# Performance work log

Measured on AMD Instinct MI355X. Metric: run time of the kernel, lower is better.

## Reference

```python
import jax, jax.numpy as jnp
import numpy as np

B = 16384
DENSE = 64
N_OH, N_MH = 8, 4
VOCAB = 100000
EMB = 32
HIST = 20
IN_DIM = DENSE + N_OH * EMB + N_MH * EMB  # 448
HID = [1024, 512, 256]
CROSS_ORDER = 4


def setup_inputs() -> dict:
    key = jax.random.key(0)
    ks = jax.random.split(key, 16)
    inp = {}
    inp['dense_x'] = jax.random.normal(ks[0], (B, DENSE), dtype=jnp.float32)
    inp['one_hot_x'] = jax.random.randint(ks[1], (B, N_OH), 0, VOCAB)
    inp['multi_hot_x'] = jax.random.randint(ks[2], (B, N_MH, HIST), 0, VOCAB)
    # embedding tables (one per field)
    inp['one_hot_emb'] = jax.random.normal(ks[3], (N_OH, VOCAB, EMB), dtype=jnp.float32) * 0.01
    inp['multi_hot_emb'] = jax.random.normal(ks[4], (N_MH, VOCAB, EMB), dtype=jnp.float32) * 0.01
    # cross layer params: w (in_dim,) per layer (xavier-like), b (in_dim,) zeros in torch init -> small random here
    inp['cross_w'] = jax.random.normal(ks[5], (CROSS_ORDER, IN_DIM), dtype=jnp.float32) * (6.0 / (IN_DIM + 1)) ** 0.5
    inp['cross_b'] = jnp.zeros((CROSS_ORDER, IN_DIM), dtype=jnp.float32)
    # deep net
    inp['W1'] = jax.random.normal(ks[6], (IN_DIM, HID[0]), dtype=jnp.float32) * (1.0 / IN_DIM) ** 0.5
    inp['b1'] = jnp.zeros((HID[0],), dtype=jnp.float32)
    inp['W2'] = jax.random.normal(ks[7], (HID[0], HID[1]), dtype=jnp.float32) * (1.0 / HID[0]) ** 0.5
    inp['b2'] = jnp.zeros((HID[1],), dtype=jnp.float32)
    inp['W3'] = jax.random.normal(ks[8], (HID[1], HID[2]), dtype=jnp.float32) * (1.0 / HID[1]) ** 0.5
    inp['b3'] = jnp.zeros((HID[2],), dtype=jnp.float32)
    inp['lin_w'] = jax.random.normal(ks[9], (IN_DIM + HID[2], 1), dtype=jnp.float32) * (1.0 / (IN_DIM + HID[2])) ** 0.5
    inp['lin_b'] = jnp.zeros((1,), dtype=jnp.float32)
    return inp


def _embed_concat(one_hot_x, multi_hot_x, one_hot_emb, multi_hot_emb):
    # per-field one-hot lookup: (B, N_OH, EMB)
    oh = jax.vmap(lambda tab, idx: tab[idx], in_axes=(0, 1), out_axes=1)(one_hot_emb, one_hot_x)
    # per-field multi-hot sum-pool: (B, N_MH, EMB)
    mh = jax.vmap(lambda tab, idx: tab[idx].sum(axis=1), in_axes=(0, 1), out_axes=1)(multi_hot_emb, multi_hot_x)
    b = one_hot_x.shape[0]
    return jnp.concatenate([oh.reshape(b, -1), mh.reshape(b, -1)], axis=1)


def _forward(dense_x, one_hot_x, multi_hot_x, one_hot_emb, multi_hot_emb,
             cross_w, cross_b, W1, b1, W2, b2, W3, b3, lin_w, lin_b):
    emb_x = _embed_concat(one_hot_x, multi_hot_x, one_hot_emb, multi_hot_emb)
    x0 = jnp.concatenate([dense_x, emb_x], axis=1)  # (B, IN_DIM)
    # CrossNet: (x0 xi^T) w == x0 * (xi . w); same math as torch bmm, O(d) form
    xi = x0
    for l in range(CROSS_ORDER):
        xi = x0 * (xi @ cross_w[l])[:, None] + cross_b[l] + xi
    # DeepNet
    h = jax.nn.relu(x0 @ W1 + b1)
    h = jax.nn.relu(h @ W2 + b2)
    h = jax.nn.relu(h @ W3 + b3)
    h_cat = jnp.concatenate([xi, h], axis=1)
    return jax.nn.sigmoid(h_cat @ lin_w + lin_b)  # (B, 1)


def reference(dense_x, one_hot_x, multi_hot_x, one_hot_emb, multi_hot_emb,
              cross_w, cross_b, W1, b1, W2, b2, W3, b3, lin_w, lin_b):
    return _forward(dense_x, one_hot_x, multi_hot_x, one_hot_emb, multi_hot_emb,
                    cross_w, cross_b, W1, b1, W2, b2, W3, b3, lin_w, lin_b)
```

## Files before the change

### kernel.cpp

```cpp
#include <hip/hip_runtime.h>
#include <hip/hip_bf16.h>
#include <math.h>

#define B_SZ 16384
#define DENSE 64
#define N_OH 8
#define N_MH 4
#define VOCAB 100000
#define EMB 32
#define HIST 20
#define IN_DIM 448
#define HID1 1024
#define HID2 512
#define HID3 256
#define CROSS_ORDER 4

typedef __bf16 bf16_t;
typedef __bf16 bf16x8 __attribute__((ext_vector_type(8)));
typedef __bf16 bf16x4 __attribute__((ext_vector_type(4)));
typedef float f32x16 __attribute__((ext_vector_type(16)));
typedef __attribute__((address_space(1))) const void cgvoid;
typedef __attribute__((address_space(3))) void lvoid;

#define S1 (IN_DIM * HID1)
#define S2 (HID1 * HID2)
#define S3 (HID2 * HID3)
#define EMB_BLOCKS (B_SZ / 4)
#define TR_BLOCKS ((S1 + S2 + S3 + 255) / 256)

__global__ __launch_bounds__(256) void embed_cross_transpose_kernel(
    const float* __restrict__ dense, const int* __restrict__ oh_idx,
    const int* __restrict__ mh_idx, const float* __restrict__ oh_emb,
    const float* __restrict__ mh_emb, const float* __restrict__ cw,
    const float* __restrict__ cb, const float* __restrict__ lw,
    const float* __restrict__ W1, const float* __restrict__ W2,
    const float* __restrict__ W3, bf16_t* __restrict__ T1,
    bf16_t* __restrict__ T2, bf16_t* __restrict__ T3,
    bf16_t* __restrict__ x0b, float* __restrict__ partial) {
  __shared__ float ldsAll[4 * IN_DIM];
  int bid = blockIdx.x;
  if (bid >= EMB_BLOCKS) {
    int idx = (bid - EMB_BLOCKS) * 256 + threadIdx.x;
    if (idx < S1) {
      int n = idx / IN_DIM, k = idx - n * IN_DIM;
      T1[idx] = (bf16_t)W1[(size_t)k * HID1 + n];
    } else if (idx < S1 + S2) {
      int i = idx - S1;
      int n = i / HID1, k = i - n * HID1;
      T2[i] = (bf16_t)W2[(size_t)k * HID2 + n];
    } else if (idx < S1 + S2 + S3) {
      int i = idx - S1 - S2;
      int n = i / HID2, k = i - n * HID2;
      T3[i] = (bf16_t)W3[(size_t)k * HID3 + n];
    }
    return;
  }
  int wv = threadIdx.x >> 6;
  int lane = threadIdx.x & 63;
  int row = bid * 4 + wv;
  float* L = ldsAll + wv * IN_DIM;

  L[lane] = dense[(size_t)row * DENSE + lane];

  {
    int f = lane >> 3, d4 = (lane & 7) * 4;
    int idx = oh_idx[row * N_OH + f];
    float4 ov = *reinterpret_cast<const float4*>(
        &oh_emb[((size_t)f * VOCAB + idx) * EMB + d4]);
    *reinterpret_cast<float4*>(&L[64 + lane * 4]) = ov;
  }

  {
    int f = lane >> 4, sub = lane & 15;
    int par = sub >> 3, d4 = (sub & 7) * 4;
    const int* hist = mh_idx + ((size_t)row * N_MH + f) * HIST;
    float4 ms = make_float4(0.f, 0.f, 0.f, 0.f);
#pragma unroll
    for (int jj = 0; jj < 10; ++jj) {
      int idx = hist[jj * 2 + par];
      float4 v = *reinterpret_cast<const float4*>(
          &mh_emb[((size_t)f * VOCAB + idx) * EMB + d4]);
      ms.x += v.x; ms.y += v.y; ms.z += v.z; ms.w += v.w;
    }
    ms.x += __shfl_xor(ms.x, 8);
    ms.y += __shfl_xor(ms.y, 8);
    ms.z += __shfl_xor(ms.z, 8);
    ms.w += __shfl_xor(ms.w, 8);
    if (par == 0)
      *reinterpret_cast<float4*>(&L[320 + f * 32 + (sub & 7) * 4]) = ms;
  }

  if (lane < 56) {
    float4 a = *reinterpret_cast<float4*>(&L[lane * 8]);
    float4 b = *reinterpret_cast<float4*>(&L[lane * 8 + 4]);
    bf16x8 o;
    o[0] = (bf16_t)a.x; o[1] = (bf16_t)a.y; o[2] = (bf16_t)a.z; o[3] = (bf16_t)a.w;
    o[4] = (bf16_t)b.x; o[5] = (bf16_t)b.y; o[6] = (bf16_t)b.z; o[7] = (bf16_t)b.w;
    *reinterpret_cast<bf16x8*>(x0b + (size_t)row * IN_DIM + lane * 8) = o;
  }

  float x0v[7], xiv[7];
#pragma unroll
  for (int r = 0; r < 7; ++r) {
    x0v[r] = L[lane + r * 64];
    xiv[r] = x0v[r];
  }
  for (int l = 0; l < CROSS_ORDER; ++l) {
    const float* w = cw + l * IN_DIM;
    const float* b = cb + l * IN_DIM;
    float dot = 0.f;
#pragma unroll
    for (int r = 0; r < 7; ++r) dot += xiv[r] * w[lane + r * 64];
#pragma unroll
    for (int s = 32; s > 0; s >>= 1) dot += __shfl_xor(dot, s);
#pragma unroll
    for (int r = 0; r < 7; ++r) xiv[r] = x0v[r] * dot + b[lane + r * 64] + xiv[r];
  }

  float s = 0.f;
#pragma unroll
  for (int r = 0; r < 7; ++r) s += xiv[r] * lw[lane + r * 64];
#pragma unroll
  for (int t = 32; t > 0; t >>= 1) s += __shfl_xor(s, t);
  if (lane == 0) partial[row] = s;
}

template <int N, int K, int GX, bool RELU>
__global__ __launch_bounds__(256) void gemm_bf16_kernel(
    const bf16_t* __restrict__ A, const bf16_t* __restrict__ Bt,
    const float* __restrict__ bias, bf16_t* __restrict__ C) {
  __shared__ bf16_t As[128 * 64];
  __shared__ bf16_t Bs[128 * 64];
  const int tid = threadIdx.x;
  const int lane = tid & 63;
  const int wid = tid >> 6;
  const int wr = wid >> 1;
  const int wc = wid & 1;

  const int nwg = gridDim.x;
  const int bid = blockIdx.x;
  const int swz = (bid & 7) * (nwg >> 3) + (bid >> 3);
  const int row0 = (swz / GX) * 128;
  const int col0 = (swz % GX) * 128;
  constexpr size_t Kb = (size_t)K * 2;

  const int l31 = lane & 31;
  const int lh = lane >> 5;

  const int strow = tid >> 3;
  const int stkb0 = (tid * 16) & 127;

  f32x16 acc[2][2];
#pragma unroll
  for (int m = 0; m < 2; ++m)
#pragma unroll
    for (int n = 0; n < 2; ++n)
#pragma unroll
      for (int r = 0; r < 16; ++r) acc[m][n][r] = 0.f;

  for (int k0 = 0; k0 < K; k0 += 64) {
    __syncthreads();
#pragma unroll
    for (int c = 0; c < 4; ++c) {
      int trow = c * 32 + strow;
      int skb = stkb0 ^ ((trow & 7) << 4);
      const char* gA = (const char*)A + (size_t)(row0 + trow) * Kb + (size_t)k0 * 2 + skb;
      const char* gB = (const char*)Bt + (size_t)(col0 + trow) * Kb + (size_t)k0 * 2 + skb;
      __builtin_amdgcn_global_load_lds((cgvoid*)gA,
          (lvoid*)((char*)As + c * 4096 + wid * 1024), 16, 0, 0);
      __builtin_amdgcn_global_load_lds((cgvoid*)gB,
          (lvoid*)((char*)Bs + c * 4096 + wid * 1024), 16, 0, 0);
    }
    __syncthreads();

#pragma unroll
    for (int kh = 0; kh < 4; ++kh) {
      const int koff = kh * 32 + lh * 16;
      bf16x8 a[2], b[2];
#pragma unroll
      for (int m = 0; m < 2; ++m) {
        int r = wr * 64 + m * 32 + l31;
        a[m] = *reinterpret_cast<const bf16x8*>(
            (const char*)As + r * 128 + (koff ^ ((r & 7) << 4)));
      }
#pragma unroll
      for (int n = 0; n < 2; ++n) {
        int ccol = wc * 64 + n * 32 + l31;
        b[n] = *reinterpret_cast<const bf16x8*>(
            (const char*)Bs + ccol * 128 + (koff ^ ((ccol & 7) << 4)));
      }
#pragma unroll
      for (int m = 0; m < 2; ++m)
#pragma unroll
        for (int n = 0; n < 2; ++n)
          acc[m][n] = __builtin_amdgcn_mfma_f32_32x32x16_bf16(a[m], b[n], acc[m][n], 0, 0, 0);
    }
  }

#pragma unroll
  for (int n = 0; n < 2; ++n) {
    int col = col0 + wc * 64 + n * 32 + l31;
    float bv = bias[col];
#pragma unroll
    for (int m = 0; m < 2; ++m) {
#pragma unroll
      for (int r = 0; r < 16; ++r) {
        int row = row0 + wr * 64 + m * 32 + (r & 3) + 8 * (r >> 2) + 4 * lh;
        float v = acc[m][n][r] + bv;
        if (RELU) v = fmaxf(v, 0.f);
        C[(size_t)row * N + col] = (bf16_t)v;
      }
    }
  }
}

__global__ __launch_bounds__(256) void final_kernel(
    const float* __restrict__ partial, const bf16_t* __restrict__ h3,
    const float* __restrict__ lw, const float* __restrict__ lb,
    float* __restrict__ out) {
  int wave = (blockIdx.x * blockDim.x + threadIdx.x) >> 6;
  int lane = threadIdx.x & 63;
  if (wave >= B_SZ) return;
  bf16x4 hv = *reinterpret_cast<const bf16x4*>(h3 + (size_t)wave * HID3 + lane * 4);
  float4 wv = *reinterpret_cast<const float4*>(lw + IN_DIM + lane * 4);
  float s = (float)hv[0] * wv.x + (float)hv[1] * wv.y +
            (float)hv[2] * wv.z + (float)hv[3] * wv.w;
#pragma unroll
  for (int t = 32; t > 0; t >>= 1) s += __shfl_xor(s, t);
  if (lane == 0) out[wave] = 1.f / (1.f + expf(-(s + partial[wave] + lb[0])));
}

extern "C" void kernel_launch(void* const* d_in, const int* in_sizes, int n_in,
                              void* d_out, int out_size, void* d_ws, size_t ws_size,
                              hipStream_t stream) {
  const float* dense = (const float*)d_in[0];
  const int* oh_idx = (const int*)d_in[1];
  const int* mh_idx = (const int*)d_in[2];
  const float* oh_emb = (const float*)d_in[3];
  const float* mh_emb = (const float*)d_in[4];
  const float* cw = (const float*)d_in[5];
  const float* cb = (const float*)d_in[6];
  const float* W1 = (const float*)d_in[7];
  const float* b1 = (const float*)d_in[8];
  const float* W2 = (const float*)d_in[9];
  const float* b2 = (const float*)d_in[10];
  const float* W3 = (const float*)d_in[11];
  const float* b3 = (const float*)d_in[12];
  const float* lw = (const float*)d_in[13];
  const float* lb = (const float*)d_in[14];
  float* out = (float*)d_out;

  char* p = (char*)d_ws;
  bf16_t* x0b = (bf16_t*)p;  p += (size_t)B_SZ * IN_DIM * 2;
  bf16_t* h1b = (bf16_t*)p;  p += (size_t)B_SZ * HID1 * 2;
  bf16_t* h2b = (bf16_t*)p;  p += (size_t)B_SZ * HID2 * 2;
  bf16_t* h3b = (bf16_t*)p;  p += (size_t)B_SZ * HID3 * 2;
  bf16_t* wT1 = (bf16_t*)p;  p += (size_t)HID1 * IN_DIM * 2;
  bf16_t* wT2 = (bf16_t*)p;  p += (size_t)HID2 * HID1 * 2;
  bf16_t* wT3 = (bf16_t*)p;  p += (size_t)HID2 * HID3 * 2;
  float* partial = (float*)p; p += (size_t)B_SZ * 4;

  embed_cross_transpose_kernel<<<EMB_BLOCKS + TR_BLOCKS, 256, 0, stream>>>(
      dense, oh_idx, mh_idx, oh_emb, mh_emb, cw, cb, lw,
      W1, W2, W3, wT1, wT2, wT3, x0b, partial);

  gemm_bf16_kernel<HID1, IN_DIM, HID1 / 128, true>
      <<<(B_SZ / 128) * (HID1 / 128), 256, 0, stream>>>(x0b, wT1, b1, h1b);
  gemm_bf16_kernel<HID2, HID1, HID2 / 128, true>
      <<<(B_SZ / 128) * (HID2 / 128), 256, 0, stream>>>(h1b, wT2, b2, h2b);
  gemm_bf16_kernel<HID3, HID2, HID3 / 128, true>
      <<<(B_SZ / 128) * (HID3 / 128), 256, 0, stream>>>(h2b, wT3, b3, h3b);

  final_kernel<<<B_SZ / 4, 256, 0, stream>>>(partial, h3b, lw, lb, out);
}
```

Baseline: 102.2 us.

## Fuse third GEMM with final linear projection and sigmoid

Replaces the third layer GEMM and the separate final kernel with one kernel. Each block computes a 64-row by full-256-column tile, applies bias and ReLU, dots with the linear weights in registers, reduces across lanes and waves through shared memory, and writes the sigmoid output. This removes the h3 round trip through global memory and one launch. In exchange it uses a different tile shape (64x256, 256 blocks), which may lower occupancy or MFMA efficiency for this layer.

```diff
diff --git a/kernel.cpp b/kernel.cpp
--- a/kernel.cpp
+++ b/kernel.cpp
@@ -17,7 +17,6 @@
 
 typedef __bf16 bf16_t;
 typedef __bf16 bf16x8 __attribute__((ext_vector_type(8)));
-typedef __bf16 bf16x4 __attribute__((ext_vector_type(4)));
 typedef float f32x16 __attribute__((ext_vector_type(16)));
 typedef __attribute__((address_space(1))) const void cgvoid;
 typedef __attribute__((address_space(3))) void lvoid;
@@ -125,7 +124,7 @@
   if (lane == 0) partial[row] = s;
 }
 
-template <int N, int K, int GX, bool RELU>
+template <int N, int K, int GX>
 __global__ __launch_bounds__(256) void gemm_bf16_kernel(
     const bf16_t* __restrict__ A, const bf16_t* __restrict__ Bt,
     const float* __restrict__ bias, bf16_t* __restrict__ C) {
@@ -206,28 +205,112 @@
 #pragma unroll
       for (int r = 0; r < 16; ++r) {
         int row = row0 + wr * 64 + m * 32 + (r & 3) + 8 * (r >> 2) + 4 * lh;
-        float v = acc[m][n][r] + bv;
-        if (RELU) v = fmaxf(v, 0.f);
+        float v = fmaxf(acc[m][n][r] + bv, 0.f);
         C[(size_t)row * N + col] = (bf16_t)v;
       }
     }
   }
 }
 
-__global__ __launch_bounds__(256) void final_kernel(
-    const float* __restrict__ partial, const bf16_t* __restrict__ h3,
-    const float* __restrict__ lw, const float* __restrict__ lb,
+__global__ __launch_bounds__(256) void gemm3_final_kernel(
+    const bf16_t* __restrict__ A,
+    const bf16_t* __restrict__ Bt,
+    const float* __restrict__ bias,
+    const float* __restrict__ lw,
+    const float* __restrict__ lb,
+    const float* __restrict__ partial,
     float* __restrict__ out) {
-  int wave = (blockIdx.x * blockDim.x + threadIdx.x) >> 6;
-  int lane = threadIdx.x & 63;
-  if (wave >= B_SZ) return;
-  bf16x4 hv = *reinterpret_cast<const bf16x4*>(h3 + (size_t)wave * HID3 + lane * 4);
-  float4 wv = *reinterpret_cast<const float4*>(lw + IN_DIM + lane * 4);
-  float s = (float)hv[0] * wv.x + (float)hv[1] * wv.y +
-            (float)hv[2] * wv.z + (float)hv[3] * wv.w;
-#pragma unroll
-  for (int t = 32; t > 0; t >>= 1) s += __shfl_xor(s, t);
-  if (lane == 0) out[wave] = 1.f / (1.f + expf(-(s + partial[wave] + lb[0])));
+  constexpr int K = HID2;
+  __shared__ bf16_t As[64 * 64];
+  __shared__ bf16_t Bs[256 * 64];
+  __shared__ float rowsum[64][2];
+  const int tid = threadIdx.x;
+  const int lane = tid & 63;
+  const int wid = tid >> 6;
+  const int wr = wid >> 1;
+  const int wc = wid & 1;
+  const int nwg = gridDim.x;
+  const int bid = blockIdx.x;
+  const int swz = (bid & 7) * (nwg >> 3) + (bid >> 3);
+  const int row0 = swz * 64;
+  constexpr size_t Kb = (size_t)K * 2;
+
+  const int l31 = lane & 31;
+  const int lh = lane >> 5;
+  const int strow = tid >> 3;
+  const int stkb0 = (tid * 16) & 127;
+
+  f32x16 acc[4];
+#pragma unroll
+  for (int n = 0; n < 4; ++n)
+#pragma unroll
+    for (int r = 0; r < 16; ++r) acc[n][r] = 0.f;
+
+  for (int k0 = 0; k0 < K; k0 += 64) {
+    __syncthreads();
+#pragma unroll
+    for (int c = 0; c < 2; ++c) {
+      int trow = c * 32 + strow;
+      int skb = stkb0 ^ ((trow & 7) << 4);
+      const char* gA = (const char*)A + (size_t)(row0 + trow) * Kb + (size_t)k0 * 2 + skb;
+      __builtin_amdgcn_global_load_lds((cgvoid*)gA,
+          (lvoid*)((char*)As + c * 4096 + wid * 1024), 16, 0, 0);
+    }
+#pragma unroll
+    for (int c = 0; c < 8; ++c) {
+      int trow = c * 32 + strow;
+      int skb = stkb0 ^ ((trow & 7) << 4);
+      const char* gB = (const char*)Bt + (size_t)trow * Kb + (size_t)k0 * 2 + skb;
+      __builtin_amdgcn_global_load_lds((cgvoid*)gB,
+          (lvoid*)((char*)Bs + c * 4096 + wid * 1024), 16, 0, 0);
+    }
+    __syncthreads();
+
+#pragma unroll
+    for (int kh = 0; kh < 4; ++kh) {
+      const int koff = kh * 32 + lh * 16;
+      int ar = wr * 32 + l31;
+      bf16x8 a = *reinterpret_cast<const bf16x8*>(
+          (const char*)As + ar * 128 + (koff ^ ((ar & 7) << 4)));
+      bf16x8 b[4];
+#pragma unroll
+      for (int n = 0; n < 4; ++n) {
+        int bc = wc * 128 + n * 32 + l31;
+        b[n] = *reinterpret_cast<const bf16x8*>(
+            (const char*)Bs + bc * 128 + (koff ^ ((bc & 7) << 4)));
+      }
+#pragma unroll
+      for (int n = 0; n < 4; ++n)
+        acc[n] = __builtin_amdgcn_mfma_f32_32x32x16_bf16(a, b[n], acc[n], 0, 0, 0);
+    }
+  }
+
+  float bv[4], wv[4];
+#pragma unroll
+  for (int n = 0; n < 4; ++n) {
+    int col = wc * 128 + n * 32 + l31;
+    bv[n] = bias[col];
+    wv[n] = lw[IN_DIM + col];
+  }
+#pragma unroll
+  for (int r = 0; r < 16; ++r) {
+    float v = 0.f;
+#pragma unroll
+    for (int n = 0; n < 4; ++n) {
+      float h = fmaxf(acc[n][r] + bv[n], 0.f);
+      v += h * wv[n];
+    }
+#pragma unroll
+    for (int t = 16; t > 0; t >>= 1) v += __shfl_xor(v, t);
+    if (l31 == 0)
+      rowsum[wr * 32 + (r & 3) + 8 * (r >> 2) + 4 * lh][wc] = v;
+  }
+  __syncthreads();
+  if (tid < 64) {
+    int grow = row0 + tid;
+    float s = rowsum[tid][0] + rowsum[tid][1] + partial[grow] + lb[0];
+    out[grow] = 1.f / (1.f + expf(-s));
+  }
 }
 
 extern "C" void kernel_launch(void* const* d_in, const int* in_sizes, int n_in,
@@ -254,7 +337,6 @@
   bf16_t* x0b = (bf16_t*)p;  p += (size_t)B_SZ * IN_DIM * 2;
   bf16_t* h1b = (bf16_t*)p;  p += (size_t)B_SZ * HID1 * 2;
   bf16_t* h2b = (bf16_t*)p;  p += (size_t)B_SZ * HID2 * 2;
-  bf16_t* h3b = (bf16_t*)p;  p += (size_t)B_SZ * HID3 * 2;
   bf16_t* wT1 = (bf16_t*)p;  p += (size_t)HID1 * IN_DIM * 2;
   bf16_t* wT2 = (bf16_t*)p;  p += (size_t)HID2 * HID1 * 2;
   bf16_t* wT3 = (bf16_t*)p;  p += (size_t)HID2 * HID3 * 2;
@@ -264,12 +346,11 @@
       dense, oh_idx, mh_idx, oh_emb, mh_emb, cw, cb, lw,
       W1, W2, W3, wT1, wT2, wT3, x0b, partial);
 
-  gemm_bf16_kernel<HID1, IN_DIM, HID1 / 128, true>
+  gemm_bf16_kernel<HID1, IN_DIM, HID1 / 128>
       <<<(B_SZ / 128) * (HID1 / 128), 256, 0, stream>>>(x0b, wT1, b1, h1b);
-  gemm_bf16_kernel<HID2, HID1, HID2 / 128, true>
+  gemm_bf16_kernel<HID2, HID1, HID2 / 128>
       <<<(B_SZ / 128) * (HID2 / 128), 256, 0, stream>>>(h1b, wT2, b2, h2b);
-  gemm_bf16_kernel<HID3, HID2, HID3 / 128, true>
-      <<<(B_SZ / 128) * (HID3 / 128), 256, 0, stream>>>(h2b, wT3, b3, h3b);
-
-  final_kernel<<<B_SZ / 4, 256, 0, stream>>>(partial, h3b, lw, lb, out);
+
+  gemm3_final_kernel<<<B_SZ / 64, 256, 0, stream>>>(
+      h2b, wT3, b3, lw, lb, partial, out);
 }
```

Result: no change. 101.2 us (-1.0%).
